# Optimization experiments

Measured on AMD Instinct MI355X. Metric: run time of the kernel, lower is better.

The kernel has to match this reference:

```python
import jax, jax.numpy as jnp
import numpy as np

NPOINT, RADIUS, SIGMA, K = 1024, 0.1, 0.05, 32
KDE_K = 128  # N_points default of kernel_density_estimation_ball


def setup_inputs() -> dict:
    key = jax.random.key(0)
    ks = jax.random.split(key, 9)
    B, N, C = 4, 4096, 16

    def glorot(k, shape):
        fan_in, fan_out = shape
        return jax.random.normal(k, shape, jnp.float32) * jnp.sqrt(2.0 / (fan_in + fan_out))

    return {
        'xyz': jax.random.uniform(ks[0], (B, N, 3), jnp.float32),      # unit cube
        'feature': jax.random.normal(ks[1], (B, N, C), jnp.float32),
        'w_mlp0': glorot(ks[2], (3 + C, 128)),
        'w_mlp1': glorot(ks[3], (128, 128)),
        'w_mlp2': glorot(ks[4], (128, 256)),
        'w_wn': glorot(ks[5], (3, 32)),
        'w_nl0': glorot(ks[6], (1, 16)),
        'w_nl1': glorot(ks[7], (16, 1)),
        'w_np': glorot(ks[8], (32, 256)),
    }


def _pdist2(a, b):
    # squared pairwise distances [B, M, N]
    return (jnp.sum(a * a, -1)[:, :, None] + jnp.sum(b * b, -1)[:, None, :]
            - 2.0 * jnp.einsum('bmd,bnd->bmn', a, b))


def _fps(xyz, npoint):
    # farthest point sampling, seeded at index 0 (matches CUDA op semantics)
    B, N, _ = xyz.shape

    def step(carry, _):
        min_d, last = carry
        p = jnp.take_along_axis(xyz, last[:, None, None], axis=1)  # [B,1,3]
        d = jnp.sum((xyz - p) ** 2, -1)                            # [B,N]
        min_d = jnp.minimum(min_d, d)
        nxt = jnp.argmax(min_d, axis=1).astype(jnp.int32)
        return (min_d, nxt), nxt

    init = (jnp.full((B, N), jnp.inf, xyz.dtype), jnp.zeros((B,), jnp.int32))
    _, rest = jax.lax.scan(step, init, None, length=npoint - 1)
    return jnp.concatenate([jnp.zeros((B, 1), jnp.int32), rest.T], axis=1)  # [B,npoint]


def _ball_query(xyz, radius, k):
    # first-k-in-index-order neighbors with d2 < r^2, padded with first hit
    B, N, _ = xyz.shape
    d2 = _pdist2(xyz, xyz)
    in_ball = d2 < radius * radius                 # self always included
    j = jnp.arange(N, dtype=jnp.int32)
    keys = jnp.where(in_ball, j, j + N)            # in-ball indices sort first
    _, idx = jax.lax.top_k(-keys, k)               # k smallest keys -> positions j
    cnt = jnp.minimum(jnp.sum(in_ball, axis=-1), k)            # [B,N]
    valid = jnp.arange(k) < cnt[..., None]
    idx = jnp.where(valid, idx, idx[..., :1])
    return idx, cnt


def _kde_ball(xyz, radius, sigma, kde_k):
    idx, cnt = _ball_query(xyz, radius, kde_k)     # [B,N,kde_k], [B,N]
    b_ix = jnp.arange(xyz.shape[0])[:, None, None]
    g = xyz[b_ix, idx] - xyz[:, :, None, :]        # [B,N,kde_k,3]
    R = jnp.sqrt(jnp.float32(sigma))
    quad = jnp.sum(jnp.square(g / R), axis=-1)     # [B,N,kde_k]
    mvn = jnp.exp(-0.5 * quad - 3.0 * jnp.log(R) - 1.5 * jnp.log(2.0 * 3.1415926))
    first = mvn[..., :1]
    total = jnp.sum(mvn, axis=-1, keepdims=True)
    cntf = cnt.astype(xyz.dtype)[..., None]
    total = total - first * (jnp.float32(kde_k) - cntf)  # remove padded duplicates
    return total / cntf                             # [B,N,1]


def _knn(k, src, q):
    d2 = _pdist2(q, src)                            # [B,P,N]
    _, idx = jax.lax.top_k(-d2, k)                  # ascending distance
    return idx


def _forward(xyz, feature, w_mlp0, w_mlp1, w_mlp2, w_wn, w_nl0, w_nl1, w_np):
    B = xyz.shape[0]
    conv = lambda x, w: jax.nn.relu(jnp.einsum('bpkc,cf->bpkf', x, w))  # bias-free 1x1 conv

    fps_idx = _fps(xyz, NPOINT)
    new_xyz = jnp.take_along_axis(xyz, fps_idx[..., None], axis=1)      # [B,P,3]

    knn_idx = _knn(K, xyz, new_xyz)                                      # [B,P,K]
    b_ix = jnp.arange(B)[:, None, None]
    grouped_xyz = xyz[b_ix, knn_idx] - new_xyz[:, :, None, :]            # [B,P,K,3]
    grouped_feature = jnp.concatenate([grouped_xyz, feature[b_ix, knn_idx]], axis=-1)

    inv_density = 1.0 / _kde_ball(xyz, RADIUS, SIGMA, KDE_K)             # [B,N,1]
    grouped_density = inv_density[b_ix, knn_idx]                          # [B,P,K,1]
    density_scale = grouped_density / jnp.max(grouped_density, axis=2, keepdims=True)

    h = conv(conv(conv(grouped_feature, w_mlp0), w_mlp1), w_mlp2)        # [B,P,K,256]
    weight = conv(grouped_xyz, w_wn)                                      # [B,P,K,32]
    density_scale = conv(conv(density_scale, w_nl0), w_nl1)               # [B,P,K,1]

    pts = h * density_scale
    pts = jnp.einsum('bpkc,bpkw->bpcw', pts, weight)                      # [B,P,256,32]
    # np_conv: 1x1 kernel with stride [1, mlp[-1]] + VALID -> only c=0 slice survives
    out = jax.nn.relu(jnp.einsum('bpw,wf->bpf', pts[:, :, 0, :], w_np))   # [B,P,256]
    return new_xyz, out


def reference(xyz, feature, w_mlp0, w_mlp1, w_mlp2, w_wn, w_nl0, w_nl1, w_np):
    return _forward(xyz, feature, w_mlp0, w_mlp1, w_mlp2, w_wn, w_nl0, w_nl1, w_np)
```

## Files before the change

kernel.cpp:

```cpp
#include <hip/hip_runtime.h>
#include <math.h>

#pragma clang fp contract(off)

typedef float v2f __attribute__((ext_vector_type(2)));

__global__ __launch_bounds__(256) void prep_kernel(
    const float* __restrict__ xyz, const float* __restrict__ w0,
    const float* __restrict__ w1, const float* __restrict__ w2,
    float* __restrict__ norms, float* __restrict__ W0T,
    float* __restrict__ W1T, float* __restrict__ W2c)
{
    int t = blockIdx.x * 256 + threadIdx.x;
    if (t < 16384) {
        float x = xyz[t*3+0], y = xyz[t*3+1], z = xyz[t*3+2];
        norms[t] = (x*x + y*y) + z*z;
        int c = t >> 7, k = t & 127;
        W1T[c*128 + k] = w1[k*128 + c];
    }
    if (t < 2432) { int c = t / 19, i = t - c*19; W0T[t] = w0[i*128 + c]; }
    if (t < 128)  { W2c[t] = w2[t*256]; }
}

template<int CTRL>
__device__ __forceinline__ unsigned long long dpp_u64(unsigned long long k) {
    int lo = (int)(unsigned int)k;
    int hi = (int)(unsigned int)(k >> 32);
    int plo = __builtin_amdgcn_update_dpp(lo, lo, CTRL, 0xF, 0xF, false);
    int phi = __builtin_amdgcn_update_dpp(hi, hi, CTRL, 0xF, 0xF, false);
    return ((unsigned long long)(unsigned int)phi << 32) | (unsigned int)plo;
}
template<int CTRL>
__device__ __forceinline__ unsigned long long max_u64_dpp(unsigned long long k) {
    unsigned long long p = dpp_u64<CTRL>(k);
    return p > k ? p : k;
}
template<int CTRL>
__device__ __forceinline__ unsigned long long min_u64_dpp(unsigned long long k) {
    unsigned long long p = dpp_u64<CTRL>(k);
    return p < k ? p : k;
}

__global__ __launch_bounds__(512) void fps_kde_kernel(
    const float* __restrict__ xyz, const float* __restrict__ norms,
    float* __restrict__ new_xyz, float* __restrict__ invden)
{
    __shared__ float4 pts[4096];
    __shared__ float  nxb[3072];
    __shared__ __attribute__((aligned(16))) unsigned long long swk[2][32];
    int tid = threadIdx.x;

    if (blockIdx.x < 4) {
        int b = blockIdx.x;
        const float* Xb = xyz + b*12288;
        for (int t = tid; t < 4096; t += 512)
            pts[t] = make_float4(Xb[t*3+0], Xb[t*3+1], Xb[t*3+2], 0.0f);
        __syncthreads();
        float4 P[8];
#pragma unroll
        for (int k = 0; k < 8; ++k) P[k] = pts[k*512 + tid];
        v2f Xp[4], Yp[4], Zp[4], md2[4];
#pragma unroll
        for (int k = 0; k < 4; ++k) {
            Xp[k].x = P[k].x;  Xp[k].y = P[k+4].x;
            Yp[k].x = P[k].y;  Yp[k].y = P[k+4].y;
            Zp[k].x = P[k].z;  Zp[k].y = P[k+4].z;
            md2[k].x = INFINITY; md2[k].y = INFINITY;
        }
        float cx = pts[0].x, cy = pts[0].y, cz = pts[0].z;
        if (tid == 0) { nxb[0] = cx; nxb[1] = cy; nxb[2] = cz; }
        int buf = 0;
        for (int it = 1; it < 1024; ++it) {
            v2f cx2, cy2, cz2;
            cx2.x = cx; cx2.y = cx;
            cy2.x = cy; cy2.y = cy;
            cz2.x = cz; cz2.y = cz;
#pragma unroll
            for (int k = 0; k < 4; ++k) {
                v2f dx = Xp[k] - cx2, dy = Yp[k] - cy2, dz = Zp[k] - cz2;
                v2f dd = (dx*dx + dy*dy) + dz*dz;
                md2[k].x = fminf(md2[k].x, dd.x);
                md2[k].y = fminf(md2[k].y, dd.y);
            }
            float bv = md2[0].x; int bj = 0;
            if (md2[1].x > bv) { bv = md2[1].x; bj = 1; }
            if (md2[2].x > bv) { bv = md2[2].x; bj = 2; }
            if (md2[3].x > bv) { bv = md2[3].x; bj = 3; }
            if (md2[0].y > bv) { bv = md2[0].y; bj = 4; }
            if (md2[1].y > bv) { bv = md2[1].y; bj = 5; }
            if (md2[2].y > bv) { bv = md2[2].y; bj = 6; }
            if (md2[3].y > bv) { bv = md2[3].y; bj = 7; }
            unsigned bp = (unsigned)(bj*512 + tid);
            unsigned long long key =
                ((unsigned long long)__float_as_uint(bv) << 32) | (unsigned)(~bp);
            key = max_u64_dpp<0xB1>(key);
            key = max_u64_dpp<0x4E>(key);
            key = max_u64_dpp<0x141>(key);
            key = max_u64_dpp<0x140>(key);
            if ((tid & 15) == 0) swk[buf][tid >> 4] = key;
            __syncthreads();
            uint4 w4 = *((const uint4*)&swk[buf][(tid & 15) << 1]);
            unsigned long long kA = ((unsigned long long)w4.y << 32) | w4.x;
            unsigned long long kB = ((unsigned long long)w4.w << 32) | w4.z;
            unsigned long long kk = kA > kB ? kA : kB;
            kk = max_u64_dpp<0xB1>(kk);
            kk = max_u64_dpp<0x4E>(kk);
            kk = max_u64_dpp<0x141>(kk);
            kk = max_u64_dpp<0x140>(kk);
            int fp = (int)(~(unsigned int)kk);
            float4 c = pts[fp];
            cx = c.x; cy = c.y; cz = c.z;
            if (tid == 0) { nxb[it*3+0] = cx; nxb[it*3+1] = cy; nxb[it*3+2] = cz; }
            buf ^= 1;
        }
        __syncthreads();
        float* NX = new_xyz + b*3072;
        for (int t = tid; t < 3072; t += 512) NX[t] = nxb[t];
    } else {
        int idx = blockIdx.x - 4;
        int b = idx >> 9;
        int wave = tid >> 6, lane = tid & 63;
        int i_local = ((idx & 511) << 3) + wave;
        const float* Xb = xyz + b*12288;
        const float* Nb = norms + b*4096;
        for (int t = tid; t < 4096; t += 512)
            pts[t] = make_float4(Xb[t*3+0], Xb[t*3+1], Xb[t*3+2], Nb[t]);
        __syncthreads();
        float4 c = pts[i_local];
        const float Rv    = sqrtf(0.05f);
        const float inv_s = 1.0f / (Rv*Rv);
        const float K1    = -3.0f*logf(Rv) - 1.5f*logf(2.0f*3.1415926f);
        float csum = 0.0f; int cnt = 0;
        for (int j = lane; j < 4096; j += 64) {
            float4 q = pts[j];
            float dot = (c.x*q.x + c.y*q.y) + c.z*q.z;
            float t2 = 2.0f * dot;
            float d2 = (c.w + q.w) - t2;
            if (d2 < 0.01f) {
                float gx = q.x - c.x, gy = q.y - c.y, gz = q.z - c.z;
                float dd = (gx*gx + gy*gy) + gz*gz;
                csum += expf(-0.5f * (dd * inv_s) + K1);
                cnt  += 1;
            }
        }
#pragma unroll
        for (int m = 1; m < 64; m <<= 1) {
            csum += __shfl_xor(csum, m, 64);
            cnt  += __shfl_xor(cnt,  m, 64);
        }
        if (lane == 0) {
            float den = csum / (float)cnt;
            invden[b*4096 + i_local] = 1.0f / den;
        }
    }
}

__global__ __launch_bounds__(256) void knn_kernel(
    const float* __restrict__ xyz, const float* __restrict__ norms,
    const float* __restrict__ new_xyz, int* __restrict__ knn_idx)
{
    __shared__ unsigned sd2[4*4096];
    __shared__ int sIdx[4*32];
    int wave = threadIdx.x >> 6, lane = threadIdx.x & 63;
    int qg = blockIdx.x*4 + wave;
    int b = qg >> 10;
    const float* Q = new_xyz + qg*3;
    float qx = Q[0], qy = Q[1], qz = Q[2];
    float nq = (qx*qx + qy*qy) + qz*qz;
    const float* Xb = xyz + b*12288;
    const float* Nb = norms + b*4096;
    unsigned* d2w = sd2 + wave*4096;
    for (int j = lane; j < 4096; j += 64) {
        float x = Xb[j*3+0], y = Xb[j*3+1], z = Xb[j*3+2];
        float dot = (qx*x + qy*y) + qz*z;
        float t2 = 2.0f*dot;
        float d = (nq + Nb[j]) - t2;
        unsigned u = __float_as_uint(d);
        unsigned m = ((unsigned)((int)u >> 31)) | 0x80000000u;
        d2w[j] = u ^ m;
    }
    for (int r = 0; r < 32; ++r) {
        unsigned best = 0xFFFFFFFFu; int bj = 0;
#pragma unroll
        for (int t = 0; t < 16; ++t) {
            int jb = t*256 + lane*4;
            uint4 v = *((const uint4*)(d2w + jb));
            if (v.x < best) { best = v.x; bj = jb;   }
            if (v.y < best) { best = v.y; bj = jb+1; }
            if (v.z < best) { best = v.z; bj = jb+2; }
            if (v.w < best) { best = v.w; bj = jb+3; }
        }
        unsigned long long key = ((unsigned long long)best << 32) | (unsigned)bj;
        key = min_u64_dpp<0xB1>(key);
        key = min_u64_dpp<0x4E>(key);
        key = min_u64_dpp<0x141>(key);
        key = min_u64_dpp<0x140>(key);
        key = min_u64_dpp<0x142>(key);
        key = min_u64_dpp<0x143>(key);
        int jwin = __builtin_amdgcn_readlane((int)(unsigned)key, 63);
        if (lane == 0) { sIdx[wave*32 + r] = jwin; d2w[jwin] = 0xFFFFFFFFu; }
    }
    if (lane < 32) knn_idx[qg*32 + lane] = sIdx[wave*32 + lane];
}

__global__ __launch_bounds__(256, 2) void group_mlp_kernel(
    const float* __restrict__ xyz, const float* __restrict__ feat,
    const float* __restrict__ new_xyz, const int* __restrict__ knn_idx,
    const float* __restrict__ invden,
    const float* __restrict__ W0T, const float* __restrict__ W1T,
    const float* __restrict__ W2c, const float* __restrict__ wwn,
    const float* __restrict__ wnl0, const float* __restrict__ wnl1,
    float* __restrict__ ptsw)
{
    int row = blockIdx.x*256 + threadIdx.x;
    int k  = row & 31;
    int pg = row >> 5;
    int b  = row >> 15;
    int j  = knn_idx[row];
    const float* Xb = xyz + b*12288;
    const float* Q  = new_xyz + pg*3;
    float in[19];
    in[0] = Xb[j*3+0] - Q[0];
    in[1] = Xb[j*3+1] - Q[1];
    in[2] = Xb[j*3+2] - Q[2];
    const float4* F = (const float4*)(feat + (size_t)(b*4096 + j)*16);
    float4 f0 = F[0], f1 = F[1], f2 = F[2], f3 = F[3];
    in[3]=f0.x; in[4]=f0.y; in[5]=f0.z; in[6]=f0.w;
    in[7]=f1.x; in[8]=f1.y; in[9]=f1.z; in[10]=f1.w;
    in[11]=f2.x; in[12]=f2.y; in[13]=f2.z; in[14]=f2.w;
    in[15]=f3.x; in[16]=f3.y; in[17]=f3.z; in[18]=f3.w;

    float gd = invden[b*4096 + j];
    float mx = gd;
#pragma unroll
    for (int m = 1; m < 32; m <<= 1) mx = fmaxf(mx, __shfl_xor(mx, m, 64));
    float dsc = gd / mx;
    float sacc = 0.0f;
#pragma unroll
    for (int t = 0; t < 16; ++t)
        sacc = fmaf(fmaxf(dsc * wnl0[t], 0.0f), wnl1[t], sacc);
    float ds = fmaxf(sacc, 0.0f);

    float h1[128];
#pragma unroll
    for (int c = 0; c < 128; ++c) {
        const float* w = W0T + c*19;
        float a = in[0]*w[0];
#pragma unroll
        for (int i = 1; i < 19; ++i) a = fmaf(in[i], w[i], a);
        h1[c] = fmaxf(a, 0.0f);
    }
    float acc0 = 0.0f;
    for (int c2 = 0; c2 < 128; ++c2) {
        const float* w = W1T + c2*128;
        float a0 = 0.0f, a1 = 0.0f, a2 = 0.0f, a3 = 0.0f;
#pragma unroll
        for (int kk = 0; kk < 128; kk += 4) {
            a0 = fmaf(h1[kk+0], w[kk+0], a0);
            a1 = fmaf(h1[kk+1], w[kk+1], a1);
            a2 = fmaf(h1[kk+2], w[kk+2], a2);
            a3 = fmaf(h1[kk+3], w[kk+3], a3);
        }
        float a = (a0+a1) + (a2+a3);
        acc0 = fmaf(fmaxf(a, 0.0f), W2c[c2], acc0);
    }
    float h0 = fmaxf(acc0, 0.0f);
    float s = h0 * ds;

    float gx = in[0], gy = in[1], gz = in[2];
    float* pw = ptsw + pg*32;
#pragma unroll
    for (int w = 0; w < 32; ++w) {
        float a = gx * wwn[w];
        a = fmaf(gy, wwn[32+w], a);
        a = fmaf(gz, wwn[64+w], a);
        float part = s * fmaxf(a, 0.0f);
#pragma unroll
        for (int m = 1; m < 32; m <<= 1) part += __shfl_xor(part, m, 64);
        if (k == 0) pw[w] = part;
    }
}

__global__ __launch_bounds__(256) void final_kernel(
    const float* __restrict__ ptsw, const float* __restrict__ wnp,
    float* __restrict__ out)
{
    int pg = blockIdx.x;
    int f  = threadIdx.x;
    const float* pw = ptsw + pg*32;
    float a = 0.0f;
#pragma unroll
    for (int w = 0; w < 32; ++w) a = fmaf(pw[w], wnp[w*256+f], a);
    out[pg*256 + f] = fmaxf(a, 0.0f);
}

extern "C" void kernel_launch(void* const* d_in, const int* in_sizes, int n_in,
                              void* d_out, int out_size, void* d_ws, size_t ws_size,
                              hipStream_t stream) {
    const float* xyz  = (const float*)d_in[0];
    const float* feat = (const float*)d_in[1];
    const float* w0   = (const float*)d_in[2];
    const float* w1   = (const float*)d_in[3];
    const float* w2   = (const float*)d_in[4];
    const float* wwn  = (const float*)d_in[5];
    const float* wnl0 = (const float*)d_in[6];
    const float* wnl1 = (const float*)d_in[7];
    const float* wnp  = (const float*)d_in[8];

    float* out_all  = (float*)d_out;
    float* new_xyz  = out_all;
    float* out2     = out_all + 12288;

    char* ws = (char*)d_ws;
    float* norms  = (float*)(ws + 0);
    float* invden = (float*)(ws + 65536);
    int*   knn    = (int*)  (ws + 131072);
    float* ptsw   = (float*)(ws + 655360);
    float* W0T    = (float*)(ws + 1179648);
    float* W1T    = (float*)(ws + 1189376);
    float* W2c    = (float*)(ws + 1254912);

    prep_kernel<<<64, 256, 0, stream>>>(xyz, w0, w1, w2, norms, W0T, W1T, W2c);
    fps_kde_kernel<<<2052, 512, 0, stream>>>(xyz, norms, new_xyz, invden);
    knn_kernel<<<1024, 256, 0, stream>>>(xyz, norms, new_xyz, knn);
    group_mlp_kernel<<<512, 256, 0, stream>>>(xyz, feat, new_xyz, knn, invden,
                                              W0T, W1T, W2c, wwn, wnl0, wnl1, ptsw);
    final_kernel<<<4096, 256, 0, stream>>>(ptsw, wnp, out2);
}
```

Baseline: 955.9 us.

## Fuse final projection into group MLP kernel and branchless FPS argmax

Replaces the per-thread branchy argmax in farthest point sampling with packed 64-bit keys reduced through a balanced max tree, shortening the serial dependency chain in each of the 1023 FPS iterations. Also removes final_kernel: every lane keeps the 32 shuffle-reduced weights and computes 8 of the 256 output features directly, dropping one launch and the ptsw workspace round trip. This adds register pressure and redundant shuffles in group_mlp_kernel, and tie-breaking behaviour in the argmax may differ slightly.

```diff
diff --git a/kernel.cpp b/kernel.cpp
--- a/kernel.cpp
+++ b/kernel.cpp
@@ -40,6 +40,10 @@
     unsigned long long p = dpp_u64<CTRL>(k);
     return p < k ? p : k;
 }
+__device__ __forceinline__ unsigned long long max_u64(unsigned long long a,
+                                                      unsigned long long b) {
+    return a > b ? a : b;
+}
 
 __global__ __launch_bounds__(512) void fps_kde_kernel(
     const float* __restrict__ xyz, const float* __restrict__ norms,
@@ -67,6 +71,9 @@
             Zp[k].x = P[k].z;  Zp[k].y = P[k+4].z;
             md2[k].x = INFINITY; md2[k].y = INFINITY;
         }
+        unsigned ip[8];
+#pragma unroll
+        for (int k = 0; k < 8; ++k) ip[k] = ~((unsigned)(k*512 + tid));
         float cx = pts[0].x, cy = pts[0].y, cz = pts[0].z;
         if (tid == 0) { nxb[0] = cx; nxb[1] = cy; nxb[2] = cz; }
         int buf = 0;
@@ -82,17 +89,29 @@
                 md2[k].x = fminf(md2[k].x, dd.x);
                 md2[k].y = fminf(md2[k].y, dd.y);
             }
-            float bv = md2[0].x; int bj = 0;
-            if (md2[1].x > bv) { bv = md2[1].x; bj = 1; }
-            if (md2[2].x > bv) { bv = md2[2].x; bj = 2; }
-            if (md2[3].x > bv) { bv = md2[3].x; bj = 3; }
-            if (md2[0].y > bv) { bv = md2[0].y; bj = 4; }
-            if (md2[1].y > bv) { bv = md2[1].y; bj = 5; }
-            if (md2[2].y > bv) { bv = md2[2].y; bj = 6; }
-            if (md2[3].y > bv) { bv = md2[3].y; bj = 7; }
-            unsigned bp = (unsigned)(bj*512 + tid);
-            unsigned long long key =
-                ((unsigned long long)__float_as_uint(bv) << 32) | (unsigned)(~bp);
+            unsigned long long k0 =
+                ((unsigned long long)__float_as_uint(md2[0].x) << 32) | ip[0];
+            unsigned long long k1 =
+                ((unsigned long long)__float_as_uint(md2[1].x) << 32) | ip[1];
+            unsigned long long k2 =
+                ((unsigned long long)__float_as_uint(md2[2].x) << 32) | ip[2];
+            unsigned long long k3 =
+                ((unsigned long long)__float_as_uint(md2[3].x) << 32) | ip[3];
+            unsigned long long k4 =
+                ((unsigned long long)__float_as_uint(md2[0].y) << 32) | ip[4];
+            unsigned long long k5 =
+                ((unsigned long long)__float_as_uint(md2[1].y) << 32) | ip[5];
+            unsigned long long k6 =
+                ((unsigned long long)__float_as_uint(md2[2].y) << 32) | ip[6];
+            unsigned long long k7 =
+                ((unsigned long long)__float_as_uint(md2[3].y) << 32) | ip[7];
+            unsigned long long t01 = max_u64(k0, k1);
+            unsigned long long t23 = max_u64(k2, k3);
+            unsigned long long t45 = max_u64(k4, k5);
+            unsigned long long t67 = max_u64(k6, k7);
+            unsigned long long t03 = max_u64(t01, t23);
+            unsigned long long t47 = max_u64(t45, t67);
+            unsigned long long key = max_u64(t03, t47);
             key = max_u64_dpp<0xB1>(key);
             key = max_u64_dpp<0x4E>(key);
             key = max_u64_dpp<0x141>(key);
@@ -210,7 +229,7 @@
     const float* __restrict__ W0T, const float* __restrict__ W1T,
     const float* __restrict__ W2c, const float* __restrict__ wwn,
     const float* __restrict__ wnl0, const float* __restrict__ wnl1,
-    float* __restrict__ ptsw)
+    const float* __restrict__ wnp, float* __restrict__ out2)
 {
     int row = blockIdx.x*256 + threadIdx.x;
     int k  = row & 31;
@@ -268,7 +287,7 @@
     float s = h0 * ds;
 
     float gx = in[0], gy = in[1], gz = in[2];
-    float* pw = ptsw + pg*32;
+    float pw[32];
 #pragma unroll
     for (int w = 0; w < 32; ++w) {
         float a = gx * wwn[w];
@@ -277,21 +296,18 @@
         float part = s * fmaxf(a, 0.0f);
 #pragma unroll
         for (int m = 1; m < 32; m <<= 1) part += __shfl_xor(part, m, 64);
-        if (k == 0) pw[w] = part;
-    }
-}
-
-__global__ __launch_bounds__(256) void final_kernel(
-    const float* __restrict__ ptsw, const float* __restrict__ wnp,
-    float* __restrict__ out)
-{
-    int pg = blockIdx.x;
-    int f  = threadIdx.x;
-    const float* pw = ptsw + pg*32;
-    float a = 0.0f;
-#pragma unroll
-    for (int w = 0; w < 32; ++w) a = fmaf(pw[w], wnp[w*256+f], a);
-    out[pg*256 + f] = fmaxf(a, 0.0f);
+        pw[w] = part;
+    }
+
+    float* outq = out2 + (size_t)pg*256;
+#pragma unroll
+    for (int o = 0; o < 8; ++o) {
+        int f = o*32 + k;
+        float a = 0.0f;
+#pragma unroll
+        for (int w = 0; w < 32; ++w) a = fmaf(pw[w], wnp[w*256+f], a);
+        outq[f] = fmaxf(a, 0.0f);
+    }
 }
 
 extern "C" void kernel_launch(void* const* d_in, const int* in_sizes, int n_in,
@@ -315,15 +331,14 @@
     float* norms  = (float*)(ws + 0);
     float* invden = (float*)(ws + 65536);
     int*   knn    = (int*)  (ws + 131072);
-    float* ptsw   = (float*)(ws + 655360);
-    float* W0T    = (float*)(ws + 1179648);
-    float* W1T    = (float*)(ws + 1189376);
-    float* W2c    = (float*)(ws + 1254912);
+    float* W0T    = (float*)(ws + 655360);
+    float* W1T    = (float*)(ws + 665088);
+    float* W2c    = (float*)(ws + 730624);
 
     prep_kernel<<<64, 256, 0, stream>>>(xyz, w0, w1, w2, norms, W0T, W1T, W2c);
     fps_kde_kernel<<<2052, 512, 0, stream>>>(xyz, norms, new_xyz, invden);
     knn_kernel<<<1024, 256, 0, stream>>>(xyz, norms, new_xyz, knn);
     group_mlp_kernel<<<512, 256, 0, stream>>>(xyz, feat, new_xyz, knn, invden,
-                                              W0T, W1T, W2c, wwn, wnl0, wnl1, ptsw);
-    final_kernel<<<4096, 256, 0, stream>>>(ptsw, wnp, out2);
-}
+                                              W0T, W1T, W2c, wwn, wnl0, wnl1,
+                                              wnp, out2);
+}
```

After: 997.1 us. 1.04x slower.
